# Performance work log

Hardware: AMD Instinct MI355X
Metric: run time of the kernel (lower is better)

Reference implementation:

```python
import jax, jax.numpy as jnp
import numpy as np

B, T, D_MODEL = 2, 1024, 512
EXPAND = 2
D_INNER = D_MODEL * EXPAND
STATE = 16
K_CONV = 4


def setup_inputs() -> dict:
    key = jax.random.key(0)
    ks = jax.random.split(key, 10)
    sc = lambda k, shape: jax.random.normal(k, shape, jnp.float32) * 0.02
    return {
        "x": jax.random.normal(ks[0], (B, T, D_MODEL), jnp.float32),
        "ln_g": jnp.ones((D_MODEL,), jnp.float32),
        "ln_b": jnp.zeros((D_MODEL,), jnp.float32),
        "W_in": sc(ks[1], (2 * D_INNER, D_MODEL)),
        "conv_w": sc(ks[2], (D_INNER, 1, K_CONV)),
        "conv_b": jnp.zeros((D_INNER,), jnp.float32),
        "W_B": sc(ks[3], (STATE, D_INNER)),
        "W_C": sc(ks[4], (STATE, D_INNER)),
        "W_dt": sc(ks[5], (D_INNER, D_INNER)),
        "b_dt": jax.random.uniform(ks[6], (D_INNER,), jnp.float32, -4.0, -1.0),
        # log_A init: A_diag = -(n+1) from HiPPO, log(-A_diag) = log(n+1), broadcast over d_inner
        "log_A": jnp.broadcast_to(jnp.log(jnp.arange(1, STATE + 1, dtype=jnp.float32)), (D_INNER, STATE)),
        "W_out": sc(ks[7], (D_MODEL, D_INNER)),
    }


def _silu(v):
    return v * jax.nn.sigmoid(v)


def reference(x, ln_g, ln_b, W_in, conv_w, conv_b, W_B, W_C, W_dt, b_dt, log_A, W_out):
    residual = x
    # LayerNorm (biased variance, eps=1e-5)
    mu = x.mean(-1, keepdims=True)
    var = x.var(-1, keepdims=True)
    xn = (x - mu) * jax.lax.rsqrt(var + 1e-5) * ln_g + ln_b
    # input projection and gate split
    xz = xn @ W_in.T                      # (B,T,2*D_INNER)
    x_main, z = jnp.split(xz, 2, axis=-1)
    # depthwise causal conv1d (padding=3 then slice to T == left-pad 3)
    xc = jnp.transpose(x_main, (0, 2, 1))  # (B,D_INNER,T)
    xc = jax.lax.conv_general_dilated(
        xc, conv_w, window_strides=(1,), padding=[(K_CONV - 1, 0)],
        dimension_numbers=("NCH", "OIH", "NCH"), feature_group_count=D_INNER,
    ) + conv_b[None, :, None]
    x_main = _silu(jnp.transpose(xc, (0, 2, 1)))  # (B,T,D_INNER)
    # selective scan in fp32
    xf = x_main.astype(jnp.float32)
    Bt = xf @ W_B.T                        # (B,T,N)
    Ct = xf @ W_C.T                        # (B,T,N)
    dt = jax.nn.softplus(xf @ W_dt.T + b_dt)  # (B,T,D_INNER)
    A = -jnp.exp(log_A)                    # (D_INNER,N)
    dA = jnp.exp(A[None, None] * dt[..., None])              # (B,T,D_INNER,N)
    dBx = dt[..., None] * Bt[:, :, None, :] * xf[..., None]  # (B,T,D_INNER,N)

    def comb(c1, c2):
        a1, b1 = c1
        a2, b2 = c2
        return a1 * a2, a2 * b1 + b2

    _, h = jax.lax.associative_scan(comb, (dA, dBx), axis=1)  # h_t = dA_t*h_{t-1}+dBx_t
    y = (h * Ct[:, :, None, :]).sum(-1).astype(x.dtype)       # (B,T,D_INNER)
    out = (y * _silu(z)) @ W_out.T
    return residual + out
```

## Files before the change

### kernel.cpp

```cpp
#include <hip/hip_runtime.h>

#define T_SEQ 1024
#define DM 512
#define DI 1024
#define NS 16
#define NC 32
#define CL 32

typedef __attribute__((ext_vector_type(8))) short short8;
typedef __attribute__((ext_vector_type(4))) float f32x4;
typedef unsigned short u16;
typedef unsigned int u32;

__device__ inline float b2f(u16 u) {
    unsigned v = ((unsigned)u) << 16;
    return __builtin_bit_cast(float, v);
}
__device__ inline u16 f2b(float f) {
    unsigned u = __builtin_bit_cast(unsigned, f);
    u += 0x7fff + ((u >> 16) & 1);
    return (u16)(u >> 16);
}

__device__ inline void g2l16(const u16* g, const short* l) {
    __builtin_amdgcn_global_load_lds((const __attribute__((address_space(1))) u32*)g,
                                     (__attribute__((address_space(3))) u32*)l, 16, 0, 0);
}

template<int K> __device__ __forceinline__ void vmwait() {
    if constexpr (K == 0) asm volatile("s_waitcnt vmcnt(0)" ::: "memory");
    else if constexpr (K == 3) asm volatile("s_waitcnt vmcnt(3)" ::: "memory");
    else if constexpr (K == 4) asm volatile("s_waitcnt vmcnt(4)" ::: "memory");
}

__global__ __launch_bounds__(256) void prep_k(const float* __restrict__ Win, const float* __restrict__ Wdt,
                       const float* __restrict__ Wout, const float* __restrict__ Wb,
                       const float* __restrict__ Wc,
                       u16* __restrict__ oWin, u16* __restrict__ wCat, u16* __restrict__ oWout,
                       const float* __restrict__ x, const float* __restrict__ g,
                       const float* __restrict__ be, u16* __restrict__ xn) {
    if (blockIdx.x < 2624) {
        int i = blockIdx.x * 256 + threadIdx.x;
        const float* s; u16* d; int off;
        if (i < 262144)      { s = Win;  d = oWin;  off = i; }
        else if (i < 524288) { s = Wdt;  d = wCat;  off = i - 262144; }
        else if (i < 655360) { s = Wout; d = oWout; off = i - 524288; }
        else if (i < 659456) { s = Wb;   d = wCat + 1048576; off = i - 655360; }
        else if (i < 663552) { s = Wc;   d = wCat + 1064960; off = i - 659456; }
        else {
            u16* dz = wCat + 1081344 + (i - 663552) * 4;
            dz[0] = 0; dz[1] = 0; dz[2] = 0; dz[3] = 0;
            return;
        }
        float4 v = ((const float4*)s)[off];
        d[off * 4 + 0] = f2b(v.x);
        d[off * 4 + 1] = f2b(v.y);
        d[off * 4 + 2] = f2b(v.z);
        d[off * 4 + 3] = f2b(v.w);
        return;
    }
    int row = blockIdx.x - 2624, tid = threadIdx.x;
    float2 v = ((const float2*)(x + row * DM))[tid];
    float s = v.x + v.y, q = v.x * v.x + v.y * v.y;
    #pragma unroll
    for (int m = 1; m < 64; m <<= 1) { s += __shfl_xor(s, m); q += __shfl_xor(q, m); }
    __shared__ float ss[4], qq[4];
    if ((tid & 63) == 0) { ss[tid >> 6] = s; qq[tid >> 6] = q; }
    __syncthreads();
    s = ss[0] + ss[1] + ss[2] + ss[3];
    q = qq[0] + qq[1] + qq[2] + qq[3];
    float mu = s / DM;
    float var = q / DM - mu * mu;
    float rs = rsqrtf(var + 1e-5f);
    int c = tid * 2;
    xn[row * DM + c]     = f2b((v.x - mu) * rs * g[c] + be[c]);
    xn[row * DM + c + 1] = f2b((v.y - mu) * rs * g[c + 1] + be[c + 1]);
}

template<int BM, int BN, int NT, int EPI>
__global__ __launch_bounds__(256) void gemm_bt(const u16* __restrict__ A, int lda,
                                               const u16* __restrict__ Bw, int ldb,
                                               void* __restrict__ outp, int ldo,
                                               const float* __restrict__ extra,
                                               float* __restrict__ BtF, float* __restrict__ CtF) {
    constexpr int ASZ = BM * 64;
    constexpr int BSZ = BN * 64;
    constexpr int S = (BM + BN) / 32;
    constexpr int MI = BM / 32, NJ = BN / 32;
    __shared__ short a_sh[3 * ASZ];
    __shared__ short b_sh[3 * BSZ];
    int tid = threadIdx.x, w = tid >> 6, lane = tid & 63;
    int m0 = blockIdx.x * BM, n0 = blockIdx.y * BN;
    int wr = (w >> 1) * (BM / 2), wc = (w & 1) * (BN / 2);
    int lr = lane & 15, kg = lane >> 4;
    f32x4 acc[MI][NJ] = {};
    const u16* Abase = A + (size_t)m0 * lda;
    const u16* Bbase = Bw + (size_t)n0 * ldb;
    int lrow8 = lane >> 3;
    int cl = lane & 7;

    auto stage = [&](int buf, int kt) {
        int k0 = kt * 64;
        #pragma unroll
        for (int q = 0; q < BM / 32; ++q) {
            int rowbase = w * (BM / 4) + q * 8;
            int row = rowbase + lrow8;
            int sc = cl ^ lrow8;
            g2l16(Abase + (size_t)row * lda + k0 + sc * 8, a_sh + buf * ASZ + rowbase * 64);
        }
        #pragma unroll
        for (int q = 0; q < BN / 32; ++q) {
            int rowbase = w * (BN / 4) + q * 8;
            int row = rowbase + lrow8;
            int sc = cl ^ lrow8;
            g2l16(Bbase + (size_t)row * ldb + k0 + sc * 8, b_sh + buf * BSZ + rowbase * 64);
        }
    };

    stage(0, 0);
    stage(1, 1);
    for (int t = 0; t < NT; ++t) {
        if (t + 1 < NT) vmwait<S>();
        else vmwait<0>();
        asm volatile("s_barrier" ::: "memory");
        if (t + 2 < NT) stage((t + 2) % 3, t + 2);
        const short* as = a_sh + (t % 3) * ASZ;
        const short* bs = b_sh + (t % 3) * BSZ;
        int rs = lr & 7;
        #pragma unroll
        for (int kk = 0; kk < 2; ++kk) {
            short8 af[MI], bfr[NJ];
            #pragma unroll
            for (int i = 0; i < MI; ++i) {
                int row = wr + i * 16 + lr;
                af[i] = *(const short8*)&as[row * 64 + ((kk * 4 + kg) ^ rs) * 8];
            }
            #pragma unroll
            for (int j = 0; j < NJ; ++j) {
                int row = wc + j * 16 + lr;
                bfr[j] = *(const short8*)&bs[row * 64 + ((kk * 4 + kg) ^ rs) * 8];
            }
            #pragma unroll
            for (int i = 0; i < MI; ++i)
                #pragma unroll
                for (int j = 0; j < NJ; ++j)
                    acc[i][j] = __builtin_amdgcn_mfma_f32_16x16x32_bf16(af[i], bfr[j], acc[i][j], 0, 0, 0);
        }
    }

    int rb = (lane >> 4) * 4, cc = lane & 15;
    #pragma unroll
    for (int i = 0; i < MI; ++i) {
        #pragma unroll
        for (int j = 0; j < NJ; ++j) {
            #pragma unroll
            for (int r = 0; r < 4; ++r) {
                int row = m0 + wr + i * 16 + rb + r;
                int col = n0 + wc + j * 16 + cc;
                float v = acc[i][j][r];
                if (EPI == 0) {
                    ((u16*)outp)[(size_t)row * ldo + col] = f2b(v);
                } else if (EPI == 2) {
                    ((float*)outp)[(size_t)row * ldo + col] = v + extra[(size_t)row * ldo + col];
                } else {
                    if (col < 1024) {
                        float xx = v + extra[col];
                        float sp = (xx > 20.f) ? xx : log1pf(__expf(xx));
                        ((u16*)outp)[(size_t)row * ldo + col] = f2b(sp);
                    } else if (col < 1040) {
                        BtF[(size_t)row * NS + (col - 1024)] = v;
                    } else if (col < 1056) {
                        CtF[(size_t)row * NS + (col - 1040)] = v;
                    }
                }
            }
        }
    }
}

__global__ void conv_k(const u16* __restrict__ xz, const float* __restrict__ w,
                       const float* __restrict__ cb, u16* __restrict__ xf) {
    int idx = blockIdx.x * 256 + threadIdx.x;
    int d = idx & (DI - 1);
    int bt = idx >> 10;
    int t = bt & (T_SEQ - 1);
    float s = cb[d];
    #pragma unroll
    for (int i = 0; i < 4; ++i) {
        int tt = t - 3 + i;
        if (tt >= 0) s += w[d * 4 + i] * b2f(xz[(size_t)(bt - 3 + i) * 2048 + d]);
    }
    float sig = 1.f / (1.f + __expf(-s));
    xf[idx] = f2b(s * sig);
}

__global__ __launch_bounds__(256) void scanA(const u16* __restrict__ dt, const u16* __restrict__ xf,
                                             const float* __restrict__ Bt, const float* __restrict__ logA,
                                             float* __restrict__ Aprod, float* __restrict__ S) {
    int tid = threadIdx.x;
    int dblk = blockIdx.x & 3;
    int c = (blockIdx.x >> 2) & (NC - 1);
    int b = blockIdx.x >> 7;
    int d = dblk * 256 + tid;
    float Adn[NS], ap[NS], h[NS];
    #pragma unroll
    for (int j = 0; j < 4; ++j)
        *(float4*)&Adn[j * 4] = ((const float4*)(logA + (size_t)d * NS))[j];
    #pragma unroll
    for (int n = 0; n < NS; ++n) { Adn[n] = -__expf(Adn[n]); ap[n] = 1.f; h[n] = 0.f; }
    const u16* dtp = dt + ((size_t)b * T_SEQ + c * CL) * DI + d;
    const u16* xfp = xf + ((size_t)b * T_SEQ + c * CL) * DI + d;
    const float* Bp = Bt + ((size_t)b * T_SEQ + c * CL) * NS;
    #pragma unroll 8
    for (int i = 0; i < CL; ++i) {
        float dtv = b2f(dtp[(size_t)i * DI]);
        float xv  = b2f(xfp[(size_t)i * DI]);
        float ux = dtv * xv;
        float Bv[NS];
        #pragma unroll
        for (int j = 0; j < 4; ++j) *(float4*)&Bv[j * 4] = ((const float4*)(Bp + (size_t)i * NS))[j];
        #pragma unroll
        for (int n = 0; n < NS; ++n) {
            float dA = __expf(Adn[n] * dtv);
            h[n] = fmaf(dA, h[n], ux * Bv[n]);
            ap[n] *= dA;
        }
    }
    size_t o = ((((size_t)c * 2 + b) * DI) + d) * NS;
    #pragma unroll
    for (int j = 0; j < 4; ++j) {
        ((float4*)(Aprod + o))[j] = *(float4*)&ap[j * 4];
        ((float4*)(S + o))[j]     = *(float4*)&h[j * 4];
    }
}

__global__ __launch_bounds__(256) void scanB(const float* __restrict__ Aprod, const float* __restrict__ S,
                                             float* __restrict__ Hin) {
    int chain = blockIdx.x * 256 + threadIdx.x;
    float h = 0.f;
    #pragma unroll 8
    for (int c = 0; c < NC; ++c) {
        size_t o = (size_t)c * 32768 + chain;
        Hin[o] = h;
        h = fmaf(Aprod[o], h, S[o]);
    }
}

__global__ __launch_bounds__(256) void scanC(const u16* __restrict__ dt, const u16* __restrict__ xf,
                                             const float* __restrict__ Bt, const float* __restrict__ Ct,
                                             const float* __restrict__ logA, const float* __restrict__ Hin,
                                             const u16* __restrict__ xz, u16* __restrict__ ym) {
    int tid = threadIdx.x;
    int dblk = blockIdx.x & 3;
    int c = (blockIdx.x >> 2) & (NC - 1);
    int b = blockIdx.x >> 7;
    int d = dblk * 256 + tid;
    float Adn[NS], h[NS];
    #pragma unroll
    for (int j = 0; j < 4; ++j)
        *(float4*)&Adn[j * 4] = ((const float4*)(logA + (size_t)d * NS))[j];
    #pragma unroll
    for (int n = 0; n < NS; ++n) Adn[n] = -__expf(Adn[n]);
    size_t o = ((((size_t)c * 2 + b) * DI) + d) * NS;
    #pragma unroll
    for (int j = 0; j < 4; ++j) *(float4*)&h[j * 4] = ((const float4*)(Hin + o))[j];
    const u16* dtp = dt + ((size_t)b * T_SEQ + c * CL) * DI + d;
    const u16* xfp = xf + ((size_t)b * T_SEQ + c * CL) * DI + d;
    const float* Bp = Bt + ((size_t)b * T_SEQ + c * CL) * NS;
    const float* Cp = Ct + ((size_t)b * T_SEQ + c * CL) * NS;
    const u16* zp = xz + ((size_t)b * T_SEQ + c * CL) * 2048 + 1024 + d;
    u16* yp = ym + ((size_t)b * T_SEQ + c * CL) * DI + d;
    #pragma unroll 8
    for (int i = 0; i < CL; ++i) {
        float dtv = b2f(dtp[(size_t)i * DI]);
        float xv  = b2f(xfp[(size_t)i * DI]);
        float ux = dtv * xv;
        float Bv[NS], Cv[NS];
        #pragma unroll
        for (int j = 0; j < 4; ++j) {
            *(float4*)&Bv[j * 4] = ((const float4*)(Bp + (size_t)i * NS))[j];
            *(float4*)&Cv[j * 4] = ((const float4*)(Cp + (size_t)i * NS))[j];
        }
        float r = 0.f;
        #pragma unroll
        for (int n = 0; n < NS; ++n) {
            float dA = __expf(Adn[n] * dtv);
            h[n] = fmaf(dA, h[n], ux * Bv[n]);
            r = fmaf(h[n], Cv[n], r);
        }
        float zv = b2f(zp[(size_t)i * 2048]);
        float sz = zv / (1.f + __expf(-zv));
        yp[(size_t)i * DI] = f2b(r * sz);
    }
}

extern "C" void kernel_launch(void* const* d_in, const int* in_sizes, int n_in,
                              void* d_out, int out_size, void* d_ws, size_t ws_size,
                              hipStream_t stream) {
    const float* x     = (const float*)d_in[0];
    const float* ln_g  = (const float*)d_in[1];
    const float* ln_b  = (const float*)d_in[2];
    const float* W_in  = (const float*)d_in[3];
    const float* conv_w= (const float*)d_in[4];
    const float* conv_b= (const float*)d_in[5];
    const float* W_B   = (const float*)d_in[6];
    const float* W_C   = (const float*)d_in[7];
    const float* W_dt  = (const float*)d_in[8];
    const float* b_dt  = (const float*)d_in[9];
    const float* log_A = (const float*)d_in[10];
    const float* W_out = (const float*)d_in[11];

    char* ws = (char*)d_ws;
    u16* wInB  = (u16*)(ws + 0);
    u16* wCat  = (u16*)(ws + 2097152);
    u16* wOutB = (u16*)(ws + 4325376);
    u16* xnB   = (u16*)(ws + 5373952);
    u16* xzB   = (u16*)(ws + 7471104);
    u16* xfB   = (u16*)(ws + 15859712);
    u16* dtB   = (u16*)(ws + 20054016);
    float* BtF = (float*)(ws + 24248320);
    float* CtF = (float*)(ws + 24379392);
    u16* ymB   = (u16*)(ws + 24510464);
    float* ApF = (float*)(ws + 28704768);
    float* SF  = (float*)(ws + 32899072);
    float* HiF = (float*)(ws + 37093376);

    prep_k<<<4672, 256, 0, stream>>>(W_in, W_dt, W_out, W_B, W_C, wInB, wCat, wOutB,
                                     x, ln_g, ln_b, xnB);
    gemm_bt<64, 64, 8, 0><<<dim3(32, 32), 256, 0, stream>>>(xnB, 512, wInB, 512,
            (void*)xzB, 2048, nullptr, nullptr, nullptr);
    conv_k<<<8192, 256, 0, stream>>>(xzB, conv_w, conv_b, xfB);
    gemm_bt<64, 64, 16, 4><<<dim3(32, 17), 256, 0, stream>>>(xfB, 1024, wCat, 1024,
            (void*)dtB, 1024, b_dt, BtF, CtF);
    scanA<<<256, 256, 0, stream>>>(dtB, xfB, BtF, log_A, ApF, SF);
    scanB<<<128, 256, 0, stream>>>(ApF, SF, HiF);
    scanC<<<256, 256, 0, stream>>>(dtB, xfB, BtF, CtF, log_A, HiF, xzB, ymB);
    gemm_bt<32, 64, 16, 2><<<dim3(64, 8), 256, 0, stream>>>(ymB, 1024, wOutB, 1024,
            d_out, 512, x, nullptr, nullptr);
}
```

Baseline: 120.6 us.

## Deepen GEMM LDS pipeline to five stages and remap blocks across XCDs

```diff
diff --git a/kernel.cpp b/kernel.cpp
--- a/kernel.cpp
+++ b/kernel.cpp
@@ -28,9 +28,10 @@
 }
 
 template<int K> __device__ __forceinline__ void vmwait() {
-    if constexpr (K == 0) asm volatile("s_waitcnt vmcnt(0)" ::: "memory");
-    else if constexpr (K == 3) asm volatile("s_waitcnt vmcnt(3)" ::: "memory");
-    else if constexpr (K == 4) asm volatile("s_waitcnt vmcnt(4)" ::: "memory");
+    if constexpr (K == 0)  asm volatile("s_waitcnt vmcnt(0)" ::: "memory");
+    else if constexpr (K == 4)  asm volatile("s_waitcnt vmcnt(4)" ::: "memory");
+    else if constexpr (K == 8)  asm volatile("s_waitcnt vmcnt(8)" ::: "memory");
+    else if constexpr (K == 12) asm volatile("s_waitcnt vmcnt(12)" ::: "memory");
 }
 
 __global__ __launch_bounds__(256) void prep_k(const float* __restrict__ Win, const float* __restrict__ Wdt,
@@ -77,82 +78,79 @@
     xn[row * DM + c + 1] = f2b((v.y - mu) * rs * g[c + 1] + be[c + 1]);
 }
 
-template<int BM, int BN, int NT, int EPI>
-__global__ __launch_bounds__(256) void gemm_bt(const u16* __restrict__ A, int lda,
+template<int NT, int EPI>
+__global__ __launch_bounds__(256) void gemm_bt(int gx,
+                                               const u16* __restrict__ A, int lda,
                                                const u16* __restrict__ Bw, int ldb,
                                                void* __restrict__ outp, int ldo,
                                                const float* __restrict__ extra,
                                                float* __restrict__ BtF, float* __restrict__ CtF) {
-    constexpr int ASZ = BM * 64;
-    constexpr int BSZ = BN * 64;
-    constexpr int S = (BM + BN) / 32;
-    constexpr int MI = BM / 32, NJ = BN / 32;
-    __shared__ short a_sh[3 * ASZ];
-    __shared__ short b_sh[3 * BSZ];
+    constexpr int ASZ = 64 * 64;
+    __shared__ short a_sh[5 * ASZ];
+    __shared__ short b_sh[5 * ASZ];
+    int nwg = gridDim.x, q8 = nwg >> 3;
+    int l = (blockIdx.x & 7) * q8 + (blockIdx.x >> 3);
+    int bx = l % gx, by = l / gx;
     int tid = threadIdx.x, w = tid >> 6, lane = tid & 63;
-    int m0 = blockIdx.x * BM, n0 = blockIdx.y * BN;
-    int wr = (w >> 1) * (BM / 2), wc = (w & 1) * (BN / 2);
+    int m0 = bx * 64, n0 = by * 64;
+    int wr = (w >> 1) * 32, wc = (w & 1) * 32;
     int lr = lane & 15, kg = lane >> 4;
-    f32x4 acc[MI][NJ] = {};
+    f32x4 acc[2][2] = {};
     const u16* Abase = A + (size_t)m0 * lda;
     const u16* Bbase = Bw + (size_t)n0 * ldb;
-    int lrow8 = lane >> 3;
+    int lrow = lane >> 3;
     int cl = lane & 7;
+    int sc = cl ^ lrow;
 
     auto stage = [&](int buf, int kt) {
         int k0 = kt * 64;
         #pragma unroll
-        for (int q = 0; q < BM / 32; ++q) {
-            int rowbase = w * (BM / 4) + q * 8;
-            int row = rowbase + lrow8;
-            int sc = cl ^ lrow8;
+        for (int qq2 = 0; qq2 < 2; ++qq2) {
+            int rowbase = qq2 * 32 + w * 8;
+            int row = rowbase + lrow;
             g2l16(Abase + (size_t)row * lda + k0 + sc * 8, a_sh + buf * ASZ + rowbase * 64);
-        }
-        #pragma unroll
-        for (int q = 0; q < BN / 32; ++q) {
-            int rowbase = w * (BN / 4) + q * 8;
-            int row = rowbase + lrow8;
-            int sc = cl ^ lrow8;
-            g2l16(Bbase + (size_t)row * ldb + k0 + sc * 8, b_sh + buf * BSZ + rowbase * 64);
+            g2l16(Bbase + (size_t)row * ldb + k0 + sc * 8, b_sh + buf * ASZ + rowbase * 64);
         }
     };
 
-    stage(0, 0);
-    stage(1, 1);
+    stage(0, 0); stage(1, 1); stage(2, 2); stage(3, 3);
     for (int t = 0; t < NT; ++t) {
-        if (t + 1 < NT) vmwait<S>();
+        int rem = NT - 1 - t;
+        if (rem >= 3) vmwait<12>();
+        else if (rem == 2) vmwait<8>();
+        else if (rem == 1) vmwait<4>();
         else vmwait<0>();
-        asm volatile("s_barrier" ::: "memory");
-        if (t + 2 < NT) stage((t + 2) % 3, t + 2);
-        const short* as = a_sh + (t % 3) * ASZ;
-        const short* bs = b_sh + (t % 3) * BSZ;
+        __builtin_amdgcn_s_barrier();
+        if (t + 4 < NT) stage((t + 4) % 5, t + 4);
+        const short* as = a_sh + (t % 5) * ASZ;
+        const short* bs = b_sh + (t % 5) * ASZ;
         int rs = lr & 7;
         #pragma unroll
         for (int kk = 0; kk < 2; ++kk) {
-            short8 af[MI], bfr[NJ];
+            short8 af[2], bfr[2];
             #pragma unroll
-            for (int i = 0; i < MI; ++i) {
+            for (int i = 0; i < 2; ++i) {
                 int row = wr + i * 16 + lr;
                 af[i] = *(const short8*)&as[row * 64 + ((kk * 4 + kg) ^ rs) * 8];
             }
             #pragma unroll
-            for (int j = 0; j < NJ; ++j) {
+            for (int j = 0; j < 2; ++j) {
                 int row = wc + j * 16 + lr;
                 bfr[j] = *(const short8*)&bs[row * 64 + ((kk * 4 + kg) ^ rs) * 8];
             }
             #pragma unroll
-            for (int i = 0; i < MI; ++i)
+            for (int i = 0; i < 2; ++i)
                 #pragma unroll
-                for (int j = 0; j < NJ; ++j)
+                for (int j = 0; j < 2; ++j)
                     acc[i][j] = __builtin_amdgcn_mfma_f32_16x16x32_bf16(af[i], bfr[j], acc[i][j], 0, 0, 0);
         }
     }
 
     int rb = (lane >> 4) * 4, cc = lane & 15;
     #pragma unroll
-    for (int i = 0; i < MI; ++i) {
-        #pragma unroll
-        for (int j = 0; j < NJ; ++j) {
+    for (int i = 0; i < 2; ++i) {
+        #pragma unroll
+        for (int j = 0; j < 2; ++j) {
             #pragma unroll
             for (int r = 0; r < 4; ++r) {
                 int row = m0 + wr + i * 16 + rb + r;
@@ -327,14 +325,14 @@
 
     prep_k<<<4672, 256, 0, stream>>>(W_in, W_dt, W_out, W_B, W_C, wInB, wCat, wOutB,
                                      x, ln_g, ln_b, xnB);
-    gemm_bt<64, 64, 8, 0><<<dim3(32, 32), 256, 0, stream>>>(xnB, 512, wInB, 512,
+    gemm_bt<8, 0><<<1024, 256, 0, stream>>>(32, xnB, 512, wInB, 512,
             (void*)xzB, 2048, nullptr, nullptr, nullptr);
     conv_k<<<8192, 256, 0, stream>>>(xzB, conv_w, conv_b, xfB);
-    gemm_bt<64, 64, 16, 4><<<dim3(32, 17), 256, 0, stream>>>(xfB, 1024, wCat, 1024,
+    gemm_bt<16, 4><<<544, 256, 0, stream>>>(32, xfB, 1024, wCat, 1024,
             (void*)dtB, 1024, b_dt, BtF, CtF);
     scanA<<<256, 256, 0, stream>>>(dtB, xfB, BtF, log_A, ApF, SF);
     scanB<<<128, 256, 0, stream>>>(ApF, SF, HiF);
     scanC<<<256, 256, 0, stream>>>(dtB, xfB, BtF, CtF, log_A, HiF, xzB, ymB);
-    gemm_bt<32, 64, 16, 2><<<dim3(64, 8), 256, 0, stream>>>(ymB, 1024, wOutB, 1024,
+    gemm_bt<16, 2><<<256, 256, 0, stream>>>(32, ymB, 1024, wOutB, 1024,
             d_out, 512, x, nullptr, nullptr);
 }
```

After: 131.9 us. 1.09x slower.
